# Kernel optimization log

Hardware: AMD Instinct MI355X
Metric: run time of the kernel (lower is better)

The kernel has to match this reference:

```python
import jax, jax.numpy as jnp
import numpy as np

B, K, NS, NT = 4, 16, 4096, 16384
TEMPERATURE = 1.0


def setup_inputs() -> dict:
    key = jax.random.key(0)
    k1, k2, k3 = jax.random.split(key, 3)
    return {
        "sem_logits": jax.random.normal(k1, (B, K, NS), dtype=jnp.float32),
        "source_pos": jax.random.normal(k2, (B, 3, NS), dtype=jnp.float32),
        "target_pos": jax.random.normal(k3, (B, 3, NT), dtype=jnp.float32),
    }


def reference(sem_logits, source_pos, target_pos):
    # temperature scaling
    x = sem_logits / max(1e-06, TEMPERATURE)
    # use_max_class=True: per-point max over class logits -> [B, 1, Ns]
    src_feat = jnp.max(x, axis=1, keepdims=True)

    # nearest neighbor via squared euclidean distance (argmin matches cdist+top-1)
    t = jnp.swapaxes(target_pos, 1, 2)  # [B, Nt, 3]
    s = jnp.swapaxes(source_pos, 1, 2)  # [B, Ns, 3]
    d2 = (
        jnp.sum(t * t, axis=-1, keepdims=True)        # [B, Nt, 1]
        + jnp.sum(s * s, axis=-1)[:, None, :]          # [B, 1, Ns]
        - 2.0 * jnp.einsum("bnd,bmd->bnm", t, s)      # [B, Nt, Ns]
    )
    nn_idx = jnp.argmin(d2, axis=-1)  # [B, Nt]

    # gather: torch's source_feat[batch_idx, :, nn_idx] yields [B, Nt, C]
    gathered = jnp.take_along_axis(src_feat, nn_idx[:, None, :], axis=2)  # [B, 1, Nt]
    out = jnp.swapaxes(gathered, 1, 2)  # [B, Nt, 1]
    return jax.nn.sigmoid(out)
```

## Files before the change

### kernel.cpp

```cpp
#include <hip/hip_runtime.h>
#include <math.h>
#include <float.h>

#define BATCH 4
#define KCLS 16
#define NSRC 4096
#define NTGT 16384

#define K2_THREADS 512
#define K2_WAVES 8
#define K2_TGT_PER_BLOCK 128
#define K2_SRC_PER_STRIPE (NSRC / K2_WAVES)

__global__ __launch_bounds__(64) void prep_kernel(
    const float* __restrict__ sem_logits,
    const float* __restrict__ source_pos,
    float4* __restrict__ src4,
    float* __restrict__ gate)
{
    int gid = blockIdx.x * blockDim.x + threadIdx.x;
    int b = gid / NSRC;
    int s = gid - b * NSRC;

    const float* lp = sem_logits + (size_t)b * KCLS * NSRC + s;
    float m = lp[0];
#pragma unroll
    for (int k = 1; k < KCLS; ++k) m = fmaxf(m, lp[(size_t)k * NSRC]);
    gate[gid] = 1.0f / (1.0f + expf(-m));

    const float* sp = source_pos + (size_t)b * 3 * NSRC + s;
    float sx = sp[0], sy = sp[NSRC], sz = sp[2 * NSRC];
    float ss = __fadd_rn(__fadd_rn(__fmul_rn(sx, sx), __fmul_rn(sy, sy)),
                         __fmul_rn(sz, sz));
    src4[gid] = make_float4(sx, sy, sz, ss);
}

__global__ __launch_bounds__(K2_THREADS) void nn_gate_kernel(
    const float4* __restrict__ src4,
    const float* __restrict__ gate,
    const float* __restrict__ target_pos,
    float* __restrict__ out)
{
    __shared__ float4 ls[NSRC];

    int tid = threadIdx.x;
    int lane = tid & 63;
    int wave = tid >> 6;

    const int blocksPerBatch = NTGT / K2_TGT_PER_BLOCK;
    int b = blockIdx.x / blocksPerBatch;
    int tbase = (blockIdx.x - b * blocksPerBatch) * K2_TGT_PER_BLOCK;

    const float4* gsrc = src4 + (size_t)b * NSRC;
#pragma unroll
    for (int i = 0; i < NSRC / K2_THREADS; ++i)
        ls[tid + i * K2_THREADS] = gsrc[tid + i * K2_THREADS];

    const float* tp = target_pos + (size_t)b * 3 * NTGT;
    int t0 = tbase + lane, t1 = tbase + 64 + lane;
    float tx0 = tp[t0], ty0 = tp[NTGT + t0], tz0 = tp[2 * NTGT + t0];
    float tx1 = tp[t1], ty1 = tp[NTGT + t1], tz1 = tp[2 * NTGT + t1];
    float tt0 = __fadd_rn(__fadd_rn(__fmul_rn(tx0, tx0), __fmul_rn(ty0, ty0)),
                          __fmul_rn(tz0, tz0));
    float tt1 = __fadd_rn(__fadd_rn(__fmul_rn(tx1, tx1), __fmul_rn(ty1, ty1)),
                          __fmul_rn(tz1, tz1));

    __syncthreads();

    const int ibase = wave * K2_SRC_PER_STRIPE;
    float best0 = FLT_MAX, best1 = FLT_MAX;
    int bi0 = 0, bi1 = 0;
#pragma unroll 4
    for (int i = 0; i < K2_SRC_PER_STRIPE; ++i) {
        float4 f = ls[ibase + i];
        float acc0 = __fmul_rn(tx0, f.x);
        acc0 = __fmaf_rn(ty0, f.y, acc0);
        acc0 = __fmaf_rn(tz0, f.z, acc0);
        float d20 = __fmaf_rn(-2.0f, acc0, __fadd_rn(tt0, f.w));
        if (d20 < best0) { best0 = d20; bi0 = i; }
        float acc1 = __fmul_rn(tx1, f.x);
        acc1 = __fmaf_rn(ty1, f.y, acc1);
        acc1 = __fmaf_rn(tz1, f.z, acc1);
        float d21 = __fmaf_rn(-2.0f, acc1, __fadd_rn(tt1, f.w));
        if (d21 < best1) { best1 = d21; bi1 = i; }
    }

    __syncthreads();

    float* smin = (float*)ls;
    int* sidx = (int*)ls + K2_WAVES * K2_TGT_PER_BLOCK;
    smin[wave * K2_TGT_PER_BLOCK + lane] = best0;
    sidx[wave * K2_TGT_PER_BLOCK + lane] = ibase + bi0;
    smin[wave * K2_TGT_PER_BLOCK + 64 + lane] = best1;
    sidx[wave * K2_TGT_PER_BLOCK + 64 + lane] = ibase + bi1;
    __syncthreads();

    if (tid < K2_TGT_PER_BLOCK) {
        float m = smin[tid];
        int mi = sidx[tid];
#pragma unroll
        for (int j = 1; j < K2_WAVES; ++j) {
            float mj = smin[j * K2_TGT_PER_BLOCK + tid];
            int ij = sidx[j * K2_TGT_PER_BLOCK + tid];
            if (mj < m || (mj == m && ij < mi)) { m = mj; mi = ij; }
        }
        out[(size_t)b * NTGT + tbase + tid] = gate[(size_t)b * NSRC + mi];
    }
}

extern "C" void kernel_launch(void* const* d_in, const int* in_sizes, int n_in,
                              void* d_out, int out_size, void* d_ws, size_t ws_size,
                              hipStream_t stream) {
    const float* sem_logits = (const float*)d_in[0];
    const float* source_pos = (const float*)d_in[1];
    const float* target_pos = (const float*)d_in[2];
    float* out = (float*)d_out;

    float4* src4 = (float4*)d_ws;
    float* gate = (float*)((char*)d_ws + sizeof(float4) * BATCH * NSRC);

    prep_kernel<<<(BATCH * NSRC) / 64, 64, 0, stream>>>(sem_logits, source_pos, src4, gate);
    nn_gate_kernel<<<BATCH * (NTGT / K2_TGT_PER_BLOCK), K2_THREADS, 0, stream>>>(
        src4, gate, target_pos, out);
}
```

Baseline: 111.9 us.

## Fuse prep into NN kernel with chunked LDS staging and lazy gate

Drops the separate prep kernel. Each block now builds packed source coordinates and squared norms straight into LDS, in two 2048-point chunks, so the LDS footprint halves and more blocks can fit per CU. The class-max and sigmoid are computed only for each target's winning neighbour, read directly from the logits. The cost is redundant norm computation in every block, an extra pair of barriers per chunk, and scattered reads of 16 logits per output.

```diff
diff --git a/kernel.cpp b/kernel.cpp
--- a/kernel.cpp
+++ b/kernel.cpp
@@ -7,54 +7,28 @@
 #define NSRC 4096
 #define NTGT 16384
 
-#define K2_THREADS 512
-#define K2_WAVES 8
-#define K2_TGT_PER_BLOCK 128
-#define K2_SRC_PER_STRIPE (NSRC / K2_WAVES)
+#define THREADS 512
+#define WAVES 8
+#define TGT_PER_BLOCK 128
+#define CHUNK 2048
+#define NCHUNK (NSRC / CHUNK)
+#define STRIPE (CHUNK / WAVES)
 
-__global__ __launch_bounds__(64) void prep_kernel(
+__global__ __launch_bounds__(THREADS) void fused_kernel(
     const float* __restrict__ sem_logits,
     const float* __restrict__ source_pos,
-    float4* __restrict__ src4,
-    float* __restrict__ gate)
-{
-    int gid = blockIdx.x * blockDim.x + threadIdx.x;
-    int b = gid / NSRC;
-    int s = gid - b * NSRC;
-
-    const float* lp = sem_logits + (size_t)b * KCLS * NSRC + s;
-    float m = lp[0];
-#pragma unroll
-    for (int k = 1; k < KCLS; ++k) m = fmaxf(m, lp[(size_t)k * NSRC]);
-    gate[gid] = 1.0f / (1.0f + expf(-m));
-
-    const float* sp = source_pos + (size_t)b * 3 * NSRC + s;
-    float sx = sp[0], sy = sp[NSRC], sz = sp[2 * NSRC];
-    float ss = __fadd_rn(__fadd_rn(__fmul_rn(sx, sx), __fmul_rn(sy, sy)),
-                         __fmul_rn(sz, sz));
-    src4[gid] = make_float4(sx, sy, sz, ss);
-}
-
-__global__ __launch_bounds__(K2_THREADS) void nn_gate_kernel(
-    const float4* __restrict__ src4,
-    const float* __restrict__ gate,
     const float* __restrict__ target_pos,
     float* __restrict__ out)
 {
-    __shared__ float4 ls[NSRC];
+    __shared__ float4 ls[CHUNK];
 
     int tid = threadIdx.x;
     int lane = tid & 63;
     int wave = tid >> 6;
 
-    const int blocksPerBatch = NTGT / K2_TGT_PER_BLOCK;
+    const int blocksPerBatch = NTGT / TGT_PER_BLOCK;
     int b = blockIdx.x / blocksPerBatch;
-    int tbase = (blockIdx.x - b * blocksPerBatch) * K2_TGT_PER_BLOCK;
-
-    const float4* gsrc = src4 + (size_t)b * NSRC;
-#pragma unroll
-    for (int i = 0; i < NSRC / K2_THREADS; ++i)
-        ls[tid + i * K2_THREADS] = gsrc[tid + i * K2_THREADS];
+    int tbase = (blockIdx.x - b * blocksPerBatch) * TGT_PER_BLOCK;
 
     const float* tp = target_pos + (size_t)b * 3 * NTGT;
     int t0 = tbase + lane, t1 = tbase + 64 + lane;
@@ -65,46 +39,68 @@
     float tt1 = __fadd_rn(__fadd_rn(__fmul_rn(tx1, tx1), __fmul_rn(ty1, ty1)),
                           __fmul_rn(tz1, tz1));
 
-    __syncthreads();
+    const float* sx = source_pos + (size_t)b * 3 * NSRC;
+    const float* sy = sx + NSRC;
+    const float* sz = sx + 2 * NSRC;
 
-    const int ibase = wave * K2_SRC_PER_STRIPE;
     float best0 = FLT_MAX, best1 = FLT_MAX;
     int bi0 = 0, bi1 = 0;
-#pragma unroll 4
-    for (int i = 0; i < K2_SRC_PER_STRIPE; ++i) {
-        float4 f = ls[ibase + i];
-        float acc0 = __fmul_rn(tx0, f.x);
-        acc0 = __fmaf_rn(ty0, f.y, acc0);
-        acc0 = __fmaf_rn(tz0, f.z, acc0);
-        float d20 = __fmaf_rn(-2.0f, acc0, __fadd_rn(tt0, f.w));
-        if (d20 < best0) { best0 = d20; bi0 = i; }
-        float acc1 = __fmul_rn(tx1, f.x);
-        acc1 = __fmaf_rn(ty1, f.y, acc1);
-        acc1 = __fmaf_rn(tz1, f.z, acc1);
-        float d21 = __fmaf_rn(-2.0f, acc1, __fadd_rn(tt1, f.w));
-        if (d21 < best1) { best1 = d21; bi1 = i; }
+
+    for (int c = 0; c < NCHUNK; ++c) {
+        __syncthreads();
+        int cg = c * CHUNK;
+#pragma unroll
+        for (int j = 0; j < CHUNK / THREADS; ++j) {
+            int s = tid + j * THREADS;
+            float x = sx[cg + s], y = sy[cg + s], z = sz[cg + s];
+            float ss = __fadd_rn(__fadd_rn(__fmul_rn(x, x), __fmul_rn(y, y)),
+                                 __fmul_rn(z, z));
+            ls[s] = make_float4(x, y, z, ss);
+        }
+        __syncthreads();
+
+        int lbase = wave * STRIPE;
+        int gbase = cg + lbase;
+#pragma unroll 8
+        for (int i = 0; i < STRIPE; ++i) {
+            float4 f = ls[lbase + i];
+            float acc0 = __fmul_rn(tx0, f.x);
+            acc0 = __fmaf_rn(ty0, f.y, acc0);
+            acc0 = __fmaf_rn(tz0, f.z, acc0);
+            float d20 = __fmaf_rn(-2.0f, acc0, __fadd_rn(tt0, f.w));
+            if (d20 < best0) { best0 = d20; bi0 = gbase + i; }
+            float acc1 = __fmul_rn(tx1, f.x);
+            acc1 = __fmaf_rn(ty1, f.y, acc1);
+            acc1 = __fmaf_rn(tz1, f.z, acc1);
+            float d21 = __fmaf_rn(-2.0f, acc1, __fadd_rn(tt1, f.w));
+            if (d21 < best1) { best1 = d21; bi1 = gbase + i; }
+        }
     }
 
     __syncthreads();
 
     float* smin = (float*)ls;
-    int* sidx = (int*)ls + K2_WAVES * K2_TGT_PER_BLOCK;
-    smin[wave * K2_TGT_PER_BLOCK + lane] = best0;
-    sidx[wave * K2_TGT_PER_BLOCK + lane] = ibase + bi0;
-    smin[wave * K2_TGT_PER_BLOCK + 64 + lane] = best1;
-    sidx[wave * K2_TGT_PER_BLOCK + 64 + lane] = ibase + bi1;
+    int* sidx = (int*)ls + WAVES * TGT_PER_BLOCK;
+    smin[wave * TGT_PER_BLOCK + lane] = best0;
+    sidx[wave * TGT_PER_BLOCK + lane] = bi0;
+    smin[wave * TGT_PER_BLOCK + 64 + lane] = best1;
+    sidx[wave * TGT_PER_BLOCK + 64 + lane] = bi1;
     __syncthreads();
 
-    if (tid < K2_TGT_PER_BLOCK) {
+    if (tid < TGT_PER_BLOCK) {
         float m = smin[tid];
         int mi = sidx[tid];
 #pragma unroll
-        for (int j = 1; j < K2_WAVES; ++j) {
-            float mj = smin[j * K2_TGT_PER_BLOCK + tid];
-            int ij = sidx[j * K2_TGT_PER_BLOCK + tid];
+        for (int j = 1; j < WAVES; ++j) {
+            float mj = smin[j * TGT_PER_BLOCK + tid];
+            int ij = sidx[j * TGT_PER_BLOCK + tid];
             if (mj < m || (mj == m && ij < mi)) { m = mj; mi = ij; }
         }
-        out[(size_t)b * NTGT + tbase + tid] = gate[(size_t)b * NSRC + mi];
+        const float* lg = sem_logits + (size_t)b * KCLS * NSRC + mi;
+        float mm = lg[0];
+#pragma unroll
+        for (int k = 1; k < KCLS; ++k) mm = fmaxf(mm, lg[(size_t)k * NSRC]);
+        out[(size_t)b * NTGT + tbase + tid] = 1.0f / (1.0f + expf(-mm));
     }
 }
 
@@ -116,10 +112,6 @@
     const float* target_pos = (const float*)d_in[2];
     float* out = (float*)d_out;
 
-    float4* src4 = (float4*)d_ws;
-    float* gate = (float*)((char*)d_ws + sizeof(float4) * BATCH * NSRC);
-
-    prep_kernel<<<(BATCH * NSRC) / 64, 64, 0, stream>>>(sem_logits, source_pos, src4, gate);
-    nn_gate_kernel<<<BATCH * (NTGT / K2_TGT_PER_BLOCK), K2_THREADS, 0, stream>>>(
-        src4, gate, target_pos, out);
+    fused_kernel<<<BATCH * (NTGT / TGT_PER_BLOCK), THREADS, 0, stream>>>(
+        sem_logits, source_pos, target_pos, out);
 }
```

Result: faster. 107.5 us (-4.0%).
